# Kernel optimization log

Measured on AMD Instinct MI355X. Metric: run time of the kernel, lower is better.

The kernel has to match this reference:

```python
import jax, jax.numpy as jnp
import numpy as np

N_NODES = 100000
N_EDGES = 1600000
IN_DIM, H_DIM, OUT_DIM = 256, 128, 2
NEG_SLOPE = 0.2  # PyG GATConv default


def gat_conv(x, edge_index, W, a_src, a_dst, b):
    """Single-head PyG GATConv (heads=1, concat, add_self_loops=True)."""
    n = x.shape[0]
    loops = jnp.arange(n, dtype=edge_index.dtype)
    src = jnp.concatenate([edge_index[0], loops])  # [E+N]
    dst = jnp.concatenate([edge_index[1], loops])
    h = x @ W                                      # [N, F_out]
    # attention logits per edge: LeakyReLU(a_src.h_src + a_dst.h_dst)
    e = jax.nn.leaky_relu((h @ a_src)[src] + (h @ a_dst)[dst], NEG_SLOPE)
    # segment softmax over incoming edges of each destination node
    m = jax.ops.segment_max(e, dst, num_segments=n)
    ex = jnp.exp(e - m[dst])
    denom = jax.ops.segment_sum(ex, dst, num_segments=n)
    alpha = ex / denom[dst]                        # self-loops guarantee denom > 0
    # scatter-aggregate weighted messages
    out = jax.ops.segment_sum(h[src] * alpha[:, None], dst, num_segments=n)
    return out + b


def setup_inputs() -> dict:
    key = jax.random.key(0)
    ks = jax.random.split(key, 10)
    glorot = lambda k, shape: jax.random.normal(k, shape, dtype=jnp.float32) * jnp.sqrt(
        2.0 / (shape[0] + shape[-1])
    ).astype(jnp.float32)
    return {
        "x": jax.random.normal(ks[0], (N_NODES, IN_DIM), dtype=jnp.float32),
        "edge_index": jax.random.randint(ks[1], (2, N_EDGES), 0, N_NODES, dtype=jnp.int64 if jax.config.jax_enable_x64 else jnp.int32),
        "W1": glorot(ks[2], (IN_DIM, H_DIM)),
        "a1_src": glorot(ks[3], (H_DIM,)),
        "a1_dst": glorot(ks[4], (H_DIM,)),
        "b1": jnp.zeros((H_DIM,), dtype=jnp.float32),
        "W2": glorot(ks[5], (H_DIM, OUT_DIM)),
        "a2_src": glorot(ks[6], (OUT_DIM,)),
        "a2_dst": glorot(ks[7], (OUT_DIM,)),
        "b2": jnp.zeros((OUT_DIM,), dtype=jnp.float32),
    }


def reference(x, edge_index, W1, a1_src, a1_dst, b1, W2, a2_src, a2_dst, b2):
    h1 = jax.nn.relu(gat_conv(x, edge_index, W1, a1_src, a1_dst, b1))
    # F.dropout(p=0.5) is identity in eval mode
    return gat_conv(h1, edge_index, W2, a2_src, a2_dst, b2)
```

## Files before the change

kernel.cpp:

```cpp
#include <hip/hip_runtime.h>
#include <hip/hip_bf16.h>

#define N_NODES 100000
#define IN_DIM 256
#define H_DIM 128
#define NEG_SLOPE 0.2f

#define NBUCK 782
#define BKT_CAP 4096
#define P1_EPT 16

__device__ __forceinline__ float lrelu(float v) { return v > 0.f ? v : NEG_SLOPE * v; }
__device__ __forceinline__ float bflo(unsigned u) { return __uint_as_float(u << 16); }
__device__ __forceinline__ float bfhi(unsigned u) { return __uint_as_float(u & 0xffff0000u); }
__device__ __forceinline__ unsigned short f2bf(float f) {
    unsigned u = __float_as_uint(f);
    return (unsigned short)((u + 0x7fffu + ((u >> 16) & 1u)) >> 16);
}
__device__ __forceinline__ float rdlanef(float v, int j) {
    return __uint_as_float(__builtin_amdgcn_readlane(__float_as_uint(v), j));
}

typedef short bfrag __attribute__((ext_vector_type(8)));
typedef float f32x4 __attribute__((ext_vector_type(4)));

__global__ __launch_bounds__(512) void fused_gemm_bin1(const float* __restrict__ x,
                                                       const float* __restrict__ W,
                                                       const float* __restrict__ a_src,
                                                       const float* __restrict__ a_dst,
                                                       unsigned short* __restrict__ hb,
                                                       float* __restrict__ as1,
                                                       float* __restrict__ ad1,
                                                       const int* __restrict__ src,
                                                       const int* __restrict__ dst,
                                                       int* __restrict__ bktAlloc,
                                                       unsigned* __restrict__ tmp,
                                                       int E, int p1B) {
    __shared__ __align__(16) char smemraw[65536];
    const int tid = threadIdx.x;

    if ((int)blockIdx.x < p1B) {
        int* hist  = (int*)smemraw;
        int* basev = hist + 1024;
        int* hist2 = basev + 1024;
        hist[tid] = 0; hist[tid + 512] = 0;
        hist2[tid] = 0; hist2[tid + 512] = 0;
        __syncthreads();
        const int e0 = blockIdx.x * (512 * P1_EPT) + tid * P1_EPT;
        int sv[P1_EPT], dv[P1_EPT];
#pragma unroll
        for (int i = 0; i < P1_EPT; ++i) {
            int e = e0 + i;
            if (e < E) { sv[i] = src[e]; dv[i] = dst[e]; }
            else dv[i] = -1;
        }
#pragma unroll
        for (int i = 0; i < P1_EPT; ++i)
            if (dv[i] >= 0) atomicAdd(&hist[dv[i] >> 7], 1);
        __syncthreads();
        for (int t = tid; t < NBUCK; t += 512) {
            int c = hist[t];
            basev[t] = c ? atomicAdd(&bktAlloc[t], c) : 0;
        }
        __syncthreads();
#pragma unroll
        for (int i = 0; i < P1_EPT; ++i) {
            if (dv[i] >= 0) {
                int b = dv[i] >> 7;
                int r = atomicAdd(&hist2[b], 1);
                int pos = basev[b] + r;
                if (pos < BKT_CAP)
                    tmp[b * BKT_CAP + pos] =
                        ((unsigned)(dv[i] & 127) << 17) | (unsigned)sv[i];
            }
        }
        return;
    }

    unsigned short* lds = (unsigned short*)smemraw;
    const int w = tid >> 6;
    const int lane = tid & 63;
    const int lo = lane & 15;
    const int hi = lane >> 4;
    const int row0 = ((int)blockIdx.x - p1B) * 128;

    {
        int col = tid & 127;
        int kb = tid >> 7;
        int c7 = col & 7;
#pragma unroll
        for (int i = 0; i < 16; ++i) {
            int k0 = i * 16 + kb * 4;
            float w0 = W[(k0 + 0) * H_DIM + col];
            float w1 = W[(k0 + 1) * H_DIM + col];
            float w2 = W[(k0 + 2) * H_DIM + col];
            float w3 = W[(k0 + 3) * H_DIM + col];
            int kblk = k0 >> 3;
            int rem = k0 & 7;
            unsigned short* d = &lds[col * 256 + ((kblk ^ c7) << 3) + rem];
            d[0] = f2bf(w0); d[1] = f2bf(w1); d[2] = f2bf(w2); d[3] = f2bf(w3);
        }
    }
    __syncthreads();

    int arow = row0 + w * 16 + lo;
    if (arow >= N_NODES) arow = N_NODES - 1;
    const float* xrow = x + (size_t)arow * IN_DIM + hi * 8;

    f32x4 acc[8] = {};
#pragma unroll
    for (int kc = 0; kc < 8; ++kc) {
        float4 xa = *reinterpret_cast<const float4*>(xrow + kc * 32);
        float4 xb = *reinterpret_cast<const float4*>(xrow + kc * 32 + 4);
        bfrag a;
        a[0] = (short)f2bf(xa.x); a[1] = (short)f2bf(xa.y);
        a[2] = (short)f2bf(xa.z); a[3] = (short)f2bf(xa.w);
        a[4] = (short)f2bf(xb.x); a[5] = (short)f2bf(xb.y);
        a[6] = (short)f2bf(xb.z); a[7] = (short)f2bf(xb.w);
        int kblk = kc * 4 + hi;
#pragma unroll
        for (int c = 0; c < 8; ++c) {
            int col = c * 16 + lo;
            const bfrag b = *reinterpret_cast<const bfrag*>(
                &lds[col * 256 + ((kblk ^ (col & 7)) << 3)]);
            acc[c] = __builtin_amdgcn_mfma_f32_16x16x32_bf16(a, b, acc[c], 0, 0, 0);
        }
    }

    float asv[8], adv[8];
#pragma unroll
    for (int c = 0; c < 8; ++c) { asv[c] = a_src[c * 16 + lo]; adv[c] = a_dst[c * 16 + lo]; }
#pragma unroll
    for (int q = 0; q < 4; ++q) {
        float ps = 0.f, pd = 0.f;
#pragma unroll
        for (int c = 0; c < 8; ++c) { ps += acc[c][q] * asv[c]; pd += acc[c][q] * adv[c]; }
#pragma unroll
        for (int off = 8; off; off >>= 1) {
            ps += __shfl_xor(ps, off);
            pd += __shfl_xor(pd, off);
        }
        int grow = row0 + w * 16 + hi * 4 + q;
        if (lo == 0 && grow < N_NODES) { as1[grow] = ps; ad1[grow] = pd; }
    }

    __syncthreads();
#pragma unroll
    for (int c = 0; c < 8; ++c)
#pragma unroll
        for (int q = 0; q < 4; ++q)
            lds[(w * 16 + hi * 4 + q) * 128 + c * 16 + lo] = f2bf(acc[c][q]);
    __syncthreads();
#pragma unroll
    for (int i = 0; i < 4; ++i) {
        int idx = i * 512 + tid;
        int row = idx >> 4;
        int chunk = idx & 15;
        int grow = row0 + row;
        if (grow < N_NODES) {
            uint4 v = *reinterpret_cast<const uint4*>(&lds[row * 128 + chunk * 8]);
            *reinterpret_cast<uint4*>(&hb[(size_t)grow * H_DIM + chunk * 8]) = v;
        }
    }
}

__global__ __launch_bounds__(512) void agg1_kernel(const unsigned int* __restrict__ hbu,
                                                   const float* __restrict__ as1,
                                                   const float* __restrict__ ad1,
                                                   const unsigned* __restrict__ tmp,
                                                   const int* __restrict__ bktAlloc,
                                                   const float* __restrict__ b1,
                                                   const float* __restrict__ W2,
                                                   const float* __restrict__ a2s,
                                                   const float* __restrict__ a2d,
                                                   float* __restrict__ h2,
                                                   float* __restrict__ as2,
                                                   float* __restrict__ ad2,
                                                   unsigned* __restrict__ colG,
                                                   unsigned* __restrict__ nodeInfo) {
    __shared__ unsigned raw[BKT_CAP];
    __shared__ unsigned colL[BKT_CAP];
    __shared__ int cnt_s[128], sc_s[128], rp_s[128];
    const int b = blockIdx.x;
    const int nb0 = b << 7;
    const int tid = threadIdx.x;
    const int myCnt = min(bktAlloc[b], BKT_CAP);

    if (tid < 128) cnt_s[tid] = 0;
    __syncthreads();
    for (int i = tid; i < myCnt; i += 512) {
        unsigned e = tmp[b * BKT_CAP + i];
        raw[i] = e;
        atomicAdd(&cnt_s[e >> 17], 1);
    }
    __syncthreads();
    if (tid < 128) sc_s[tid] = cnt_s[tid];
    __syncthreads();
    for (int off = 1; off < 128; off <<= 1) {
        int u = (tid < 128 && tid >= off) ? sc_s[tid - off] : 0;
        __syncthreads();
        if (tid < 128) sc_s[tid] += u;
        __syncthreads();
    }
    if (tid < 128) { rp_s[tid] = sc_s[tid] - cnt_s[tid]; cnt_s[tid] = 0; }
    __syncthreads();
    for (int i = tid; i < myCnt; i += 512) {
        unsigned e = raw[i];
        int dl = e >> 17;
        int o = atomicAdd(&cnt_s[dl], 1);
        colL[rp_s[dl] + o] = e & 0x1FFFFu;
    }
    __syncthreads();
    for (int i = tid; i < myCnt; i += 512) colG[b * BKT_CAP + i] = colL[i];
    if (tid < 128 && nb0 + tid < N_NODES)
        nodeInfo[nb0 + tid] = ((unsigned)rp_s[tid] << 8) | (unsigned)cnt_s[tid];

    const int wv = tid >> 6;
    const int lane = tid & 63;
    float2 bb = *reinterpret_cast<const float2*>(&b1[lane * 2]);
    float4 w2 = *reinterpret_cast<const float4*>(&W2[lane * 4]);
    float a2s0 = a2s[0], a2s1 = a2s[1], a2d0 = a2d[0], a2d1 = a2d[1];

    for (int ni = wv; ni < 128; ni += 8) {
        int node = nb0 + ni;
        if (node >= N_NODES) break;
        const int beg = rp_s[ni], deg = cnt_s[ni];
        float adi = ad1[node];
        float wself = __expf(lrelu(as1[node] + adi));
        unsigned hvs = hbu[(unsigned)node * 64u + lane];
        float ax = wself * bflo(hvs), ay = wself * bfhi(hvs);
        float lsum = 0.0f;

        for (int p0 = 0; p0 < deg; p0 += 64) {
            const int jn = min(64, deg - p0);
            int s_l = (int)colL[beg + p0 + (lane < jn ? lane : 0)];
            float e_l = (lane < jn) ? __expf(lrelu(as1[s_l] + adi)) : 0.0f;
            lsum += e_l;
            int j = 0;
            for (; j + 4 <= jn; j += 4) {
                const unsigned* r0 = hbu + ((size_t)__builtin_amdgcn_readlane(s_l, j)     << 6);
                const unsigned* r1 = hbu + ((size_t)__builtin_amdgcn_readlane(s_l, j + 1) << 6);
                const unsigned* r2 = hbu + ((size_t)__builtin_amdgcn_readlane(s_l, j + 2) << 6);
                const unsigned* r3 = hbu + ((size_t)__builtin_amdgcn_readlane(s_l, j + 3) << 6);
                unsigned v0 = r0[lane];
                unsigned v1 = r1[lane];
                unsigned v2 = r2[lane];
                unsigned v3 = r3[lane];
                float w0 = rdlanef(e_l, j);
                float w1 = rdlanef(e_l, j + 1);
                float w2f = rdlanef(e_l, j + 2);
                float w3 = rdlanef(e_l, j + 3);
                ax += (w0 * bflo(v0) + w1 * bflo(v1)) + (w2f * bflo(v2) + w3 * bflo(v3));
                ay += (w0 * bfhi(v0) + w1 * bfhi(v1)) + (w2f * bfhi(v2) + w3 * bfhi(v3));
            }
            for (; j < jn; ++j) {
                const unsigned* r = hbu + ((size_t)__builtin_amdgcn_readlane(s_l, j) << 6);
                float w = rdlanef(e_l, j);
                unsigned v = r[lane];
                ax += w * bflo(v);
                ay += w * bfhi(v);
            }
        }
#pragma unroll
        for (int off = 32; off; off >>= 1) lsum += __shfl_xor(lsum, off);
        float inv = 1.0f / (lsum + wself);

        float o0 = fmaxf(ax * inv + bb.x, 0.0f);
        float o1 = fmaxf(ay * inv + bb.y, 0.0f);

        float p0 = o0 * w2.x + o1 * w2.z;
        float p1 = o0 * w2.y + o1 * w2.w;
#pragma unroll
        for (int off = 32; off; off >>= 1) {
            p0 += __shfl_xor(p0, off);
            p1 += __shfl_xor(p1, off);
        }
        if (lane == 0) {
            h2[node * 2 + 0] = p0;
            h2[node * 2 + 1] = p1;
            as2[node] = p0 * a2s0 + p1 * a2s1;
            ad2[node] = p0 * a2d0 + p1 * a2d1;
        }
    }
}

__global__ __launch_bounds__(256) void agg2_kernel(const float* __restrict__ h2,
                                                   const float* __restrict__ as2,
                                                   const float* __restrict__ ad2,
                                                   const unsigned* __restrict__ colG,
                                                   const unsigned* __restrict__ nodeInfo,
                                                   const float* __restrict__ b2,
                                                   float* __restrict__ out) {
    int node = blockIdx.x * 256 + threadIdx.x;
    if (node >= N_NODES) return;
    const float2* __restrict__ h2v = (const float2*)h2;
    unsigned info = nodeInfo[node];
    const unsigned* cp = colG + (size_t)(node >> 7) * BKT_CAP + (info >> 8);
    const int deg = (int)(info & 255u);
    float adi = ad2[node];
    float w0s = __expf(lrelu(as2[node] + adi));
    float l = w0s;
    float2 hv0 = h2v[(unsigned)node];
    float a0 = w0s * hv0.x, a1 = w0s * hv0.y;
    int p = 0;
    for (; p + 4 <= deg; p += 4) {
        unsigned s0 = cp[p], s1 = cp[p + 1], s2 = cp[p + 2], s3 = cp[p + 3];
        float w0 = __expf(lrelu(as2[s0] + adi));
        float w1 = __expf(lrelu(as2[s1] + adi));
        float w2 = __expf(lrelu(as2[s2] + adi));
        float w3 = __expf(lrelu(as2[s3] + adi));
        float2 v0 = h2v[s0];
        float2 v1 = h2v[s1];
        float2 v2 = h2v[s2];
        float2 v3 = h2v[s3];
        l += (w0 + w1) + (w2 + w3);
        a0 += (w0 * v0.x + w1 * v1.x) + (w2 * v2.x + w3 * v3.x);
        a1 += (w0 * v0.y + w1 * v1.y) + (w2 * v2.y + w3 * v3.y);
    }
    for (; p < deg; ++p) {
        unsigned s = cp[p];
        float w = __expf(lrelu(as2[s] + adi));
        float2 hv = h2v[s];
        l += w;
        a0 += w * hv.x;
        a1 += w * hv.y;
    }
    float inv = 1.0f / l;
    out[node * 2 + 0] = a0 * inv + b2[0];
    out[node * 2 + 1] = a1 * inv + b2[1];
}

static inline char* ws_bump(char*& p, size_t bytes) {
    char* r = p;
    p += (bytes + 255) & ~(size_t)255;
    return r;
}

extern "C" void kernel_launch(void* const* d_in, const int* in_sizes, int n_in,
                              void* d_out, int out_size, void* d_ws, size_t ws_size,
                              hipStream_t stream) {
    const float* x   = (const float*)d_in[0];
    const int*   ei  = (const int*)d_in[1];
    const float* W1  = (const float*)d_in[2];
    const float* a1s = (const float*)d_in[3];
    const float* a1d = (const float*)d_in[4];
    const float* b1  = (const float*)d_in[5];
    const float* W2  = (const float*)d_in[6];
    const float* a2s = (const float*)d_in[7];
    const float* a2d = (const float*)d_in[8];
    const float* b2  = (const float*)d_in[9];
    float* out = (float*)d_out;

    const int E = in_sizes[1] / 2;
    const int* src = ei;
    const int* dstp = ei + E;

    char* p = (char*)d_ws;
    unsigned short* hb = (unsigned short*)ws_bump(p, (size_t)N_NODES * H_DIM * 2);
    unsigned* tmp  = (unsigned*)ws_bump(p, (size_t)NBUCK * BKT_CAP * 4);
    unsigned* colG = (unsigned*)ws_bump(p, (size_t)NBUCK * BKT_CAP * 4);
    unsigned* nodeInfo = (unsigned*)ws_bump(p, (size_t)N_NODES * 4);
    float* as1    = (float*)ws_bump(p, (size_t)N_NODES * 4);
    float* ad1    = (float*)ws_bump(p, (size_t)N_NODES * 4);
    int*   bktAlloc = (int*)ws_bump(p, 1024 * 4);
    float* h2     = (float*)ws_bump(p, (size_t)N_NODES * 2 * 4);
    float* as2    = (float*)ws_bump(p, (size_t)N_NODES * 4);
    float* ad2    = (float*)ws_bump(p, (size_t)N_NODES * 4);

    const int nodeBlocks = (N_NODES + 255) / 256;
    const int p1Blocks = (E + 512 * P1_EPT - 1) / (512 * P1_EPT);
    const int gemmBlocks = (N_NODES + 127) / 128;

    hipMemsetAsync(bktAlloc, 0, 1024 * 4, stream);

    fused_gemm_bin1<<<p1Blocks + gemmBlocks, 512, 0, stream>>>(
        x, W1, a1s, a1d, hb, as1, ad1, src, dstp, bktAlloc, tmp, E, p1Blocks);

    agg1_kernel<<<NBUCK, 512, 0, stream>>>((const unsigned int*)hb, as1, ad1,
                                           tmp, bktAlloc, b1, W2, a2s, a2d,
                                           h2, as2, ad2, colG, nodeInfo);
    agg2_kernel<<<nodeBlocks, 256, 0, stream>>>(h2, as2, ad2, colG, nodeInfo, b2, out);
}
```

Before: 151.8 us.

## Split bucket CSR build from layer-1 aggregation; one wave per node

```diff
diff --git a/kernel.cpp b/kernel.cpp
--- a/kernel.cpp
+++ b/kernel.cpp
@@ -164,123 +164,138 @@
     }
 }
 
-__global__ __launch_bounds__(512) void agg1_kernel(const unsigned int* __restrict__ hbu,
+__global__ __launch_bounds__(512) void bin_pass2(const unsigned* __restrict__ tmp,
+                                                 const int* __restrict__ bktAlloc,
+                                                 unsigned* __restrict__ colG,
+                                                 unsigned* __restrict__ nodeInfo) {
+    __shared__ int cnt[128], sc[128], rp[128];
+    const int b = blockIdx.x;
+    const int nb0 = b << 7;
+    const int nmax = min(128, N_NODES - nb0);
+    const int tid = threadIdx.x;
+    const int myCnt = min(bktAlloc[b], BKT_CAP);
+    const unsigned* btmp = tmp + (size_t)b * BKT_CAP;
+    unsigned* bcol = colG + (size_t)b * BKT_CAP;
+
+    if (tid < 128) cnt[tid] = 0;
+    __syncthreads();
+    for (int i = tid; i < myCnt; i += 512)
+        atomicAdd(&cnt[btmp[i] >> 17], 1);
+    __syncthreads();
+    if (tid < 128) sc[tid] = cnt[tid];
+    __syncthreads();
+    for (int off = 1; off < 128; off <<= 1) {
+        int u = (tid < 128 && tid >= off) ? sc[tid - off] : 0;
+        __syncthreads();
+        if (tid < 128) sc[tid] += u;
+        __syncthreads();
+    }
+    if (tid < 128) { rp[tid] = sc[tid] - cnt[tid]; cnt[tid] = 0; }
+    __syncthreads();
+    if (tid < nmax)
+        nodeInfo[nb0 + tid] = ((unsigned)rp[tid] << 8);
+    for (int i = tid; i < myCnt; i += 512) {
+        unsigned e = btmp[i];
+        int dl = (int)(e >> 17);
+        int o = atomicAdd(&cnt[dl], 1);
+        bcol[rp[dl] + o] = e & 0x1FFFFu;
+    }
+    __syncthreads();
+    if (tid < nmax)
+        nodeInfo[nb0 + tid] = ((unsigned)rp[tid] << 8) | (unsigned)cnt[tid];
+}
+
+__global__ __launch_bounds__(256) void agg1_kernel(const unsigned int* __restrict__ hbu,
                                                    const float* __restrict__ as1,
                                                    const float* __restrict__ ad1,
-                                                   const unsigned* __restrict__ tmp,
-                                                   const int* __restrict__ bktAlloc,
+                                                   const unsigned* __restrict__ colG,
+                                                   const unsigned* __restrict__ nodeInfo,
                                                    const float* __restrict__ b1,
                                                    const float* __restrict__ W2,
                                                    const float* __restrict__ a2s,
                                                    const float* __restrict__ a2d,
                                                    float* __restrict__ h2,
                                                    float* __restrict__ as2,
-                                                   float* __restrict__ ad2,
-                                                   unsigned* __restrict__ colG,
-                                                   unsigned* __restrict__ nodeInfo) {
-    __shared__ unsigned raw[BKT_CAP];
-    __shared__ unsigned colL[BKT_CAP];
-    __shared__ int cnt_s[128], sc_s[128], rp_s[128];
-    const int b = blockIdx.x;
-    const int nb0 = b << 7;
-    const int tid = threadIdx.x;
-    const int myCnt = min(bktAlloc[b], BKT_CAP);
-
-    if (tid < 128) cnt_s[tid] = 0;
-    __syncthreads();
-    for (int i = tid; i < myCnt; i += 512) {
-        unsigned e = tmp[b * BKT_CAP + i];
-        raw[i] = e;
-        atomicAdd(&cnt_s[e >> 17], 1);
-    }
-    __syncthreads();
-    if (tid < 128) sc_s[tid] = cnt_s[tid];
-    __syncthreads();
-    for (int off = 1; off < 128; off <<= 1) {
-        int u = (tid < 128 && tid >= off) ? sc_s[tid - off] : 0;
-        __syncthreads();
-        if (tid < 128) sc_s[tid] += u;
-        __syncthreads();
-    }
-    if (tid < 128) { rp_s[tid] = sc_s[tid] - cnt_s[tid]; cnt_s[tid] = 0; }
-    __syncthreads();
-    for (int i = tid; i < myCnt; i += 512) {
-        unsigned e = raw[i];
-        int dl = e >> 17;
-        int o = atomicAdd(&cnt_s[dl], 1);
-        colL[rp_s[dl] + o] = e & 0x1FFFFu;
-    }
-    __syncthreads();
-    for (int i = tid; i < myCnt; i += 512) colG[b * BKT_CAP + i] = colL[i];
-    if (tid < 128 && nb0 + tid < N_NODES)
-        nodeInfo[nb0 + tid] = ((unsigned)rp_s[tid] << 8) | (unsigned)cnt_s[tid];
-
-    const int wv = tid >> 6;
-    const int lane = tid & 63;
+                                                   float* __restrict__ ad2) {
+    int node = blockIdx.x * 4 + (threadIdx.x >> 6);
+    int lane = threadIdx.x & 63;
+    if (node >= N_NODES) return;
+
+    unsigned info = nodeInfo[node];
+    const unsigned* ecol = colG + ((size_t)(node >> 7) * BKT_CAP + (info >> 8));
+    const int deg = (int)(info & 255u);
+
+    float adi = ad1[node];
+    float wself = __expf(lrelu(as1[node] + adi));
+    unsigned hvs = hbu[(unsigned)node * 64u + lane];
+    float ax = wself * bflo(hvs), ay = wself * bfhi(hvs);
+    float lsum = 0.0f;
+
+    for (int p0 = 0; p0 < deg; p0 += 64) {
+        const int jn = min(64, deg - p0);
+        int s_l = (int)ecol[p0 + (lane < jn ? lane : 0)];
+        float e_l = (lane < jn) ? __expf(lrelu(as1[s_l] + adi)) : 0.0f;
+        lsum += e_l;
+        int j = 0;
+        for (; j + 8 <= jn; j += 8) {
+            const unsigned* r0 = hbu + ((size_t)__builtin_amdgcn_readlane(s_l, j)     << 6);
+            const unsigned* r1 = hbu + ((size_t)__builtin_amdgcn_readlane(s_l, j + 1) << 6);
+            const unsigned* r2 = hbu + ((size_t)__builtin_amdgcn_readlane(s_l, j + 2) << 6);
+            const unsigned* r3 = hbu + ((size_t)__builtin_amdgcn_readlane(s_l, j + 3) << 6);
+            const unsigned* r4 = hbu + ((size_t)__builtin_amdgcn_readlane(s_l, j + 4) << 6);
+            const unsigned* r5 = hbu + ((size_t)__builtin_amdgcn_readlane(s_l, j + 5) << 6);
+            const unsigned* r6 = hbu + ((size_t)__builtin_amdgcn_readlane(s_l, j + 6) << 6);
+            const unsigned* r7 = hbu + ((size_t)__builtin_amdgcn_readlane(s_l, j + 7) << 6);
+            unsigned v0 = r0[lane];
+            unsigned v1 = r1[lane];
+            unsigned v2 = r2[lane];
+            unsigned v3 = r3[lane];
+            unsigned v4 = r4[lane];
+            unsigned v5 = r5[lane];
+            unsigned v6 = r6[lane];
+            unsigned v7 = r7[lane];
+            float w0 = rdlanef(e_l, j);
+            float w1 = rdlanef(e_l, j + 1);
+            float w2 = rdlanef(e_l, j + 2);
+            float w3 = rdlanef(e_l, j + 3);
+            float w4 = rdlanef(e_l, j + 4);
+            float w5 = rdlanef(e_l, j + 5);
+            float w6 = rdlanef(e_l, j + 6);
+            float w7 = rdlanef(e_l, j + 7);
+            ax += (w0 * bflo(v0) + w1 * bflo(v1)) + (w2 * bflo(v2) + w3 * bflo(v3))
+                + (w4 * bflo(v4) + w5 * bflo(v5)) + (w6 * bflo(v6) + w7 * bflo(v7));
+            ay += (w0 * bfhi(v0) + w1 * bfhi(v1)) + (w2 * bfhi(v2) + w3 * bfhi(v3))
+                + (w4 * bfhi(v4) + w5 * bfhi(v5)) + (w6 * bfhi(v6) + w7 * bfhi(v7));
+        }
+        for (; j < jn; ++j) {
+            const unsigned* r = hbu + ((size_t)__builtin_amdgcn_readlane(s_l, j) << 6);
+            float w = rdlanef(e_l, j);
+            unsigned v = r[lane];
+            ax += w * bflo(v);
+            ay += w * bfhi(v);
+        }
+    }
+#pragma unroll
+    for (int off = 32; off; off >>= 1) lsum += __shfl_xor(lsum, off);
+    float inv = 1.0f / (lsum + wself);
+
     float2 bb = *reinterpret_cast<const float2*>(&b1[lane * 2]);
+    float o0 = fmaxf(ax * inv + bb.x, 0.0f);
+    float o1 = fmaxf(ay * inv + bb.y, 0.0f);
+
     float4 w2 = *reinterpret_cast<const float4*>(&W2[lane * 4]);
-    float a2s0 = a2s[0], a2s1 = a2s[1], a2d0 = a2d[0], a2d1 = a2d[1];
-
-    for (int ni = wv; ni < 128; ni += 8) {
-        int node = nb0 + ni;
-        if (node >= N_NODES) break;
-        const int beg = rp_s[ni], deg = cnt_s[ni];
-        float adi = ad1[node];
-        float wself = __expf(lrelu(as1[node] + adi));
-        unsigned hvs = hbu[(unsigned)node * 64u + lane];
-        float ax = wself * bflo(hvs), ay = wself * bfhi(hvs);
-        float lsum = 0.0f;
-
-        for (int p0 = 0; p0 < deg; p0 += 64) {
-            const int jn = min(64, deg - p0);
-            int s_l = (int)colL[beg + p0 + (lane < jn ? lane : 0)];
-            float e_l = (lane < jn) ? __expf(lrelu(as1[s_l] + adi)) : 0.0f;
-            lsum += e_l;
-            int j = 0;
-            for (; j + 4 <= jn; j += 4) {
-                const unsigned* r0 = hbu + ((size_t)__builtin_amdgcn_readlane(s_l, j)     << 6);
-                const unsigned* r1 = hbu + ((size_t)__builtin_amdgcn_readlane(s_l, j + 1) << 6);
-                const unsigned* r2 = hbu + ((size_t)__builtin_amdgcn_readlane(s_l, j + 2) << 6);
-                const unsigned* r3 = hbu + ((size_t)__builtin_amdgcn_readlane(s_l, j + 3) << 6);
-                unsigned v0 = r0[lane];
-                unsigned v1 = r1[lane];
-                unsigned v2 = r2[lane];
-                unsigned v3 = r3[lane];
-                float w0 = rdlanef(e_l, j);
-                float w1 = rdlanef(e_l, j + 1);
-                float w2f = rdlanef(e_l, j + 2);
-                float w3 = rdlanef(e_l, j + 3);
-                ax += (w0 * bflo(v0) + w1 * bflo(v1)) + (w2f * bflo(v2) + w3 * bflo(v3));
-                ay += (w0 * bfhi(v0) + w1 * bfhi(v1)) + (w2f * bfhi(v2) + w3 * bfhi(v3));
-            }
-            for (; j < jn; ++j) {
-                const unsigned* r = hbu + ((size_t)__builtin_amdgcn_readlane(s_l, j) << 6);
-                float w = rdlanef(e_l, j);
-                unsigned v = r[lane];
-                ax += w * bflo(v);
-                ay += w * bfhi(v);
-            }
-        }
-#pragma unroll
-        for (int off = 32; off; off >>= 1) lsum += __shfl_xor(lsum, off);
-        float inv = 1.0f / (lsum + wself);
-
-        float o0 = fmaxf(ax * inv + bb.x, 0.0f);
-        float o1 = fmaxf(ay * inv + bb.y, 0.0f);
-
-        float p0 = o0 * w2.x + o1 * w2.z;
-        float p1 = o0 * w2.y + o1 * w2.w;
-#pragma unroll
-        for (int off = 32; off; off >>= 1) {
-            p0 += __shfl_xor(p0, off);
-            p1 += __shfl_xor(p1, off);
-        }
-        if (lane == 0) {
-            h2[node * 2 + 0] = p0;
-            h2[node * 2 + 1] = p1;
-            as2[node] = p0 * a2s0 + p1 * a2s1;
-            ad2[node] = p0 * a2d0 + p1 * a2d1;
-        }
+    float p0 = o0 * w2.x + o1 * w2.z;
+    float p1 = o0 * w2.y + o1 * w2.w;
+#pragma unroll
+    for (int off = 32; off; off >>= 1) {
+        p0 += __shfl_xor(p0, off);
+        p1 += __shfl_xor(p1, off);
+    }
+    if (lane == 0) {
+        h2[node * 2 + 0] = p0;
+        h2[node * 2 + 1] = p1;
+        as2[node] = p0 * a2s[0] + p1 * a2s[1];
+        ad2[node] = p0 * a2d[0] + p1 * a2d[1];
     }
 }
 
@@ -295,7 +310,7 @@
     if (node >= N_NODES) return;
     const float2* __restrict__ h2v = (const float2*)h2;
     unsigned info = nodeInfo[node];
-    const unsigned* cp = colG + (size_t)(node >> 7) * BKT_CAP + (info >> 8);
+    const unsigned* cp = colG + ((size_t)(node >> 7) * BKT_CAP + (info >> 8));
     const int deg = (int)(info & 255u);
     float adi = ad2[node];
     float w0s = __expf(lrelu(as2[node] + adi));
@@ -375,9 +390,10 @@
 
     fused_gemm_bin1<<<p1Blocks + gemmBlocks, 512, 0, stream>>>(
         x, W1, a1s, a1d, hb, as1, ad1, src, dstp, bktAlloc, tmp, E, p1Blocks);
-
-    agg1_kernel<<<NBUCK, 512, 0, stream>>>((const unsigned int*)hb, as1, ad1,
-                                           tmp, bktAlloc, b1, W2, a2s, a2d,
-                                           h2, as2, ad2, colG, nodeInfo);
+    bin_pass2<<<NBUCK, 512, 0, stream>>>(tmp, bktAlloc, colG, nodeInfo);
+
+    agg1_kernel<<<(N_NODES + 3) / 4, 256, 0, stream>>>((const unsigned int*)hb, as1, ad1,
+                                                       colG, nodeInfo, b1, W2, a2s, a2d,
+                                                       h2, as2, ad2);
     agg2_kernel<<<nodeBlocks, 256, 0, stream>>>(h2, as2, ad2, colG, nodeInfo, b2, out);
 }
```

Result: no change. 151.5 us (-0.2%).
